# Kernel tuning notes

Hardware: AMD Instinct MI355X
Metric: run time of the kernel (lower is better)

## Reference

```python
import jax, jax.numpy as jnp
import numpy as np

B, S, D, H, DH, R = 8, 2048, 1024, 16, 64, 32
ALPHA, BETA, GAMMA = 0.2, 0.1, 0.1


def setup_inputs() -> dict:
    key = jax.random.key(0)
    ks = jax.random.split(key, 5)
    x = jax.random.normal(ks[0], (B, S, D), jnp.float32)
    q = jax.random.normal(ks[1], (B, S, H, DH), jnp.float32)
    k = jax.random.normal(ks[2], (B, S, H, DH), jnp.float32)
    v_value = jax.random.normal(ks[3], (B, S, D), jnp.float32)
    # reentry_proj weight (orthogonal init approximated by scaled gaussian)
    W = jax.random.normal(ks[4], (D, D), jnp.float32) * np.float32(np.sqrt(0.5 / D))
    return {"x": x, "q": q, "k": k, "v_value": v_value, "W": W}


def _normalize(t):
    return t / (jnp.linalg.norm(t, axis=-1, keepdims=True) + 1e-6)


def reference(x, q, k, v_value, W):
    Bz, Sl, Dm = x.shape
    qf = q.reshape(Bz, Sl, Dm).transpose(1, 0, 2)        # (S, B, D)
    kf = k.reshape(Bz, Sl, Dm).transpose(1, 0, 2)        # (S, B, D)
    vf = v_value.transpose(1, 0, 2)                      # (S, B, D)
    U0 = jnp.zeros((Bz, R, Dm), x.dtype)
    V0 = jnp.zeros((Bz, R, Dm), x.dtype)

    def step(carry, inp):
        U, V = carry
        q_t, k_t, v_t = inp                              # each (B, D)
        U = (1.0 - ALPHA) * U + ALPHA * _normalize(q_t)[:, None, :]
        V = (1.0 - ALPHA) * V + ALPHA * _normalize(k_t)[:, None, :]
        # y_t = (U^T V) v_t, computed factorized: never materialize dim x dim
        s = jnp.einsum('brd,bd->br', V, v_t)             # (B, R)
        y = jnp.einsum('brd,br->bd', U, s)               # (B, D)
        n = jnp.maximum(jnp.linalg.norm(y, axis=-1, keepdims=True), 1e-6)
        y = y / (1.0 + BETA * (n - 1.0))                 # homeostasis
        fb = GAMMA * (y @ W.T)                           # reentry projection
        return (U, V), fb

    (_, _), fbs = jax.lax.scan(step, (U0, V0), (qf, kf, vf))
    return x + fbs.transpose(1, 0, 2)                    # (B, S, D)
```

## Files before the change

### kernel.cpp

```cpp
#include <hip/hip_runtime.h>
#include <hip/hip_bf16.h>
#include <cstdint>
#include <cstddef>

#define B_ 8
#define S_ 2048
#define D_ 1024
#define RFAC 32.0f
#define ALPHA 0.2f
#define BETA 0.1f
#define GAMMA 0.1f
#define KW 32
#define TB 64
#define PF_ 8

typedef float f32x4_t __attribute__((ext_vector_type(4)));
typedef short bf16x8_t __attribute__((ext_vector_type(8)));

__device__ __forceinline__ unsigned short f2bf(float f) {
    unsigned u = __float_as_uint(f);
    u = (u + 0x7fffu + ((u >> 16) & 1u)) >> 16;
    return (unsigned short)u;
}
__device__ __forceinline__ float bf2f(unsigned short h) {
    return __uint_as_float(((unsigned)h) << 16);
}

__global__ __launch_bounds__(256) void wconv_k(const float* __restrict__ W,
                                               unsigned short* __restrict__ Wb) {
    int i = blockIdx.x * 256 + threadIdx.x;
    float4 w = ((const float4*)W)[i];
    ushort4 o;
    o.x = f2bf(w.x); o.y = f2bf(w.y); o.z = f2bf(w.z); o.w = f2bf(w.w);
    ((ushort4*)Wb)[i] = o;
}

__global__ __launch_bounds__(256) void ema_fused_k(const float* __restrict__ q,
                                                   const float* __restrict__ kk,
                                                   const float* __restrict__ vv,
                                                   unsigned short* __restrict__ Ub,
                                                   float* __restrict__ coef) {
    __shared__ float smn[2][8];
    __shared__ float sm2[TB * 8];
    const int chunks = S_ / TB;
    int b  = blockIdx.x / chunks;
    int t0 = (blockIdx.x % chunks) * TB;
    int ts = t0 - KW; if (ts < 0) ts = 0;
    int tid = threadIdx.x;
    int lane = tid & 63, wave = tid >> 6;
    size_t bbase = (size_t)b * S_ * D_ + tid * 4;
    const float* qp = q + bbase;
    const float* kp = kk + bbase;
    const float* vp = vv + bbase;
    unsigned short* up = Ub + bbase;

    float4 pq[PF_], pk[PF_], pv[PF_];
#pragma unroll
    for (int j = 0; j < PF_; ++j) {
        size_t o = (size_t)(ts + j) * D_;
        pq[j] = *(const float4*)(qp + o);
        pk[j] = *(const float4*)(kp + o);
        if (ts + j >= t0) pv[j] = *(const float4*)(vp + o);
    }
    float u0 = 0.f, u1 = 0.f, u2 = 0.f, u3 = 0.f;
    float v0 = 0.f, v1 = 0.f, v2 = 0.f, v3 = 0.f;
    const float om = 1.f - ALPHA;
    const int NI = t0 + TB - ts;
    const int tend = t0 + TB;
    for (int g = 0; g < NI; g += PF_) {
#pragma unroll
        for (int j = 0; j < PF_; ++j) {
            int t = ts + g + j;
            int slot = t & 1;
            float sqq = pq[j].x * pq[j].x + pq[j].y * pq[j].y
                      + pq[j].z * pq[j].z + pq[j].w * pq[j].w;
            float sqk = pk[j].x * pk[j].x + pk[j].y * pk[j].y
                      + pk[j].z * pk[j].z + pk[j].w * pk[j].w;
#pragma unroll
            for (int off = 32; off > 0; off >>= 1) {
                sqq += __shfl_xor(sqq, off, 64);
                sqk += __shfl_xor(sqk, off, 64);
            }
            if (lane == 0) {
                smn[slot][wave * 2 + 0] = sqq;
                smn[slot][wave * 2 + 1] = sqk;
            }
            asm volatile("s_waitcnt lgkmcnt(0)" ::: "memory");
            __builtin_amdgcn_s_barrier();
            asm volatile("" ::: "memory");
            float nq = smn[slot][0] + smn[slot][2] + smn[slot][4] + smn[slot][6];
            float nk = smn[slot][1] + smn[slot][3] + smn[slot][5] + smn[slot][7];
            float aq = ALPHA / (sqrtf(nq) + 1e-6f);
            float ak = ALPHA / (sqrtf(nk) + 1e-6f);
            u0 = om * u0 + aq * pq[j].x; u1 = om * u1 + aq * pq[j].y;
            u2 = om * u2 + aq * pq[j].z; u3 = om * u3 + aq * pq[j].w;
            v0 = om * v0 + ak * pk[j].x; v1 = om * v1 + ak * pk[j].y;
            v2 = om * v2 + ak * pk[j].z; v3 = om * v3 + ak * pk[j].w;
            if (t >= t0) {
                float uu = u0 * u0 + u1 * u1 + u2 * u2 + u3 * u3;
                float sd = v0 * pv[j].x + v1 * pv[j].y + v2 * pv[j].z + v3 * pv[j].w;
#pragma unroll
                for (int off = 32; off > 0; off >>= 1) {
                    uu += __shfl_xor(uu, off, 64);
                    sd += __shfl_xor(sd, off, 64);
                }
                if (lane == 0) {
                    sm2[(t - t0) * 8 + wave * 2 + 0] = uu;
                    sm2[(t - t0) * 8 + wave * 2 + 1] = sd;
                }
                ushort4 us;
                us.x = f2bf(u0); us.y = f2bf(u1); us.z = f2bf(u2); us.w = f2bf(u3);
                *(ushort4*)(up + (size_t)t * D_) = us;
            }
            int tf = t + PF_;
            int tc = tf < tend ? tf : tend - 1;
            size_t o2 = (size_t)tc * D_;
            pq[j] = *(const float4*)(qp + o2);
            pk[j] = *(const float4*)(kp + o2);
            if (tf >= t0) pv[j] = *(const float4*)(vp + o2);
        }
    }
    __syncthreads();
    if (tid < TB) {
        float uu = sm2[tid * 8 + 0] + sm2[tid * 8 + 2] + sm2[tid * 8 + 4] + sm2[tid * 8 + 6];
        float sd = sm2[tid * 8 + 1] + sm2[tid * 8 + 3] + sm2[tid * 8 + 5] + sm2[tid * 8 + 7];
        float nrm = RFAC * fabsf(sd) * sqrtf(uu);
        float n = fmaxf(nrm, 1e-6f);
        coef[b * S_ + t0 + tid] = GAMMA * RFAC * sd / (1.f + BETA * (n - 1.f));
    }
}

#define BM 128
#define BN 128
#define BK 64
#define NT (D_ / BK)

__global__ __launch_bounds__(256) void gemm_k(const unsigned short* __restrict__ A,
                                              const unsigned short* __restrict__ Bw,
                                              const float* __restrict__ coef,
                                              const float* __restrict__ x,
                                              float* __restrict__ out) {
    const int N = D_, K = D_;
    __shared__ unsigned short lds[2 * 2 * BM * BK];
    int bid = blockIdx.x;
    int swz = (bid & 7) * 128 + (bid >> 3);
    int tm = swz >> 3, tn = swz & 7;
    int m0 = tm * BM, n0 = tn * BN;
    int tid = threadIdx.x;
    int lane = tid & 63;
    int wid = tid >> 6;
    int wr = wid >> 1, wc = wid & 1;
    int lr = lane & 15, lg = lane >> 4;

    f32x4_t acc[4][4];
#pragma unroll
    for (int i = 0; i < 4; ++i)
#pragma unroll
        for (int j = 0; j < 4; ++j)
            acc[i][j] = (f32x4_t){0.f, 0.f, 0.f, 0.f};

#define STAGE_MAT(buf, kt, isB)                                                       \
    {                                                                                 \
        const unsigned short* Gp =                                                    \
            ((isB) ? Bw + (size_t)n0 * K : A + (size_t)m0 * K) + (size_t)(kt) * BK;   \
        char* Lp = (char*)lds + (buf) * 32768 + (isB) * 16384;                        \
        _Pragma("unroll")                                                             \
        for (int i = 0; i < 4; ++i) {                                                 \
            int c = i * 256 + tid;                                                    \
            int row = c >> 3, cl = c & 7;                                             \
            int gc = cl ^ (row & 7);                   \
            __builtin_amdgcn_global_load_lds(                                         \
                (const __attribute__((address_space(1))) void*)(Gp + (size_t)row * K + gc * 8), \
                (__attribute__((address_space(3))) void*)(Lp + c * 16), 16, 0, 0);    \
        }                                                                             \
    }
#define STAGE_TILE(buf, kt) STAGE_MAT(buf, kt, 0) STAGE_MAT(buf, kt, 1)

    STAGE_TILE(0, 0);
    STAGE_TILE(1, 1);

    for (int t = 0; t < NT; ++t) {
        if (t == NT - 1) asm volatile("s_waitcnt vmcnt(0)" ::: "memory");
        else             asm volatile("s_waitcnt vmcnt(8)" ::: "memory");
        __builtin_amdgcn_s_barrier();
        const unsigned short* La = lds + (t & 1) * 16384;
        const unsigned short* Lb = La + 8192;
        bf16x8_t af[4][2], bf[4][2];
#pragma unroll
        for (int kkk = 0; kkk < 2; ++kkk) {
#pragma unroll
            for (int mi = 0; mi < 4; ++mi) {
                int row = wr * 64 + mi * 16 + lr;
                int ch = (kkk * 4 + lg) ^ (row & 7);
                af[mi][kkk] = *(const bf16x8_t*)(La + (row * 8 + ch) * 8);
            }
#pragma unroll
            for (int ni = 0; ni < 4; ++ni) {
                int row = wc * 64 + ni * 16 + lr;
                int ch = (kkk * 4 + lg) ^ (row & 7);
                bf[ni][kkk] = *(const bf16x8_t*)(Lb + (row * 8 + ch) * 8);
            }
        }
        asm volatile("s_waitcnt lgkmcnt(0)" ::: "memory");
        __builtin_amdgcn_sched_barrier(0);
        __builtin_amdgcn_s_setprio(1);
#pragma unroll
        for (int kkk = 0; kkk < 2; ++kkk)
#pragma unroll
            for (int mi = 0; mi < 4; ++mi)
#pragma unroll
                for (int ni = 0; ni < 4; ++ni)
                    acc[mi][ni] = __builtin_amdgcn_mfma_f32_16x16x32_bf16(
                        af[mi][kkk], bf[ni][kkk], acc[mi][ni], 0, 0, 0);
        __builtin_amdgcn_s_setprio(0);
        __builtin_amdgcn_s_barrier();
        if (t + 2 < NT) { STAGE_TILE((t & 1), t + 2); }
    }
#undef STAGE_TILE
#undef STAGE_MAT

#pragma unroll
    for (int mi = 0; mi < 4; ++mi) {
#pragma unroll
        for (int i = 0; i < 4; ++i) {
            int m = m0 + wr * 64 + mi * 16 + lg * 4 + i;
            float cf = coef[m];
#pragma unroll
            for (int ni = 0; ni < 4; ++ni) {
                int n = n0 + wc * 64 + ni * 16 + lr;
                size_t idx = (size_t)m * N + n;
                out[idx] = x[idx] + cf * acc[mi][ni][i];
            }
        }
    }
}

extern "C" void kernel_launch(void* const* d_in, const int* in_sizes, int n_in,
                              void* d_out, int out_size, void* d_ws, size_t ws_size,
                              hipStream_t stream) {
    const float* x  = (const float*)d_in[0];
    const float* q  = (const float*)d_in[1];
    const float* k  = (const float*)d_in[2];
    const float* vv = (const float*)d_in[3];
    const float* W  = (const float*)d_in[4];
    float* out = (float*)d_out;

    const size_t M = (size_t)B_ * S_;
    char* ws = (char*)d_ws;
    unsigned short* Ub = (unsigned short*)ws;
    unsigned short* Wb = (unsigned short*)(ws + M * D_ * 2);
    float* coef = (float*)(ws + M * D_ * 2 + (size_t)D_ * D_ * 2);
    size_t needed = M * D_ * 2 + (size_t)D_ * D_ * 2 + M * 4;
    if (ws_size < needed) return;

    wconv_k<<<dim3((D_ * D_) / 1024), dim3(256), 0, stream>>>(W, Wb);
    ema_fused_k<<<dim3(B_ * (S_ / TB)), dim3(256), 0, stream>>>(q, k, vv, Ub, coef);
    gemm_k<<<dim3((M / BM) * (D_ / BN)), dim3(256), 0, stream>>>(Ub, Wb, coef, x, out);
}
```

Measured before the change: 139.0 us.

## Compute EMA norms ahead of use and defer per-step reductions to LDS

```diff
diff --git a/kernel.cpp b/kernel.cpp
--- a/kernel.cpp
+++ b/kernel.cpp
@@ -13,6 +13,7 @@
 #define KW 32
 #define TB 64
 #define PF_ 8
+#define NS 4
 
 typedef float f32x4_t __attribute__((ext_vector_type(4)));
 typedef short bf16x8_t __attribute__((ext_vector_type(8)));
@@ -21,9 +22,6 @@
     unsigned u = __float_as_uint(f);
     u = (u + 0x7fffu + ((u >> 16) & 1u)) >> 16;
     return (unsigned short)u;
-}
-__device__ __forceinline__ float bf2f(unsigned short h) {
-    return __uint_as_float(((unsigned)h) << 16);
 }
 
 __global__ __launch_bounds__(256) void wconv_k(const float* __restrict__ W,
@@ -40,8 +38,8 @@
                                                    const float* __restrict__ vv,
                                                    unsigned short* __restrict__ Ub,
                                                    float* __restrict__ coef) {
-    __shared__ float smn[2][8];
-    __shared__ float sm2[TB * 8];
+    __shared__ float smn[8][8];
+    __shared__ float pp[TB][256][2];
     const int chunks = S_ / TB;
     int b  = blockIdx.x / chunks;
     int t0 = (blockIdx.x % chunks) * TB;
@@ -53,6 +51,7 @@
     const float* kp = kk + bbase;
     const float* vp = vv + bbase;
     unsigned short* up = Ub + bbase;
+    const int tend = t0 + TB;
 
     float4 pq[PF_], pk[PF_], pv[PF_];
 #pragma unroll
@@ -62,52 +61,60 @@
         pk[j] = *(const float4*)(kp + o);
         if (ts + j >= t0) pv[j] = *(const float4*)(vp + o);
     }
-    float u0 = 0.f, u1 = 0.f, u2 = 0.f, u3 = 0.f;
-    float v0 = 0.f, v1 = 0.f, v2 = 0.f, v3 = 0.f;
+#pragma unroll
+    for (int j = 0; j < NS; ++j) {
+        float sqq = pq[j].x*pq[j].x + pq[j].y*pq[j].y + pq[j].z*pq[j].z + pq[j].w*pq[j].w;
+        float sqk = pk[j].x*pk[j].x + pk[j].y*pk[j].y + pk[j].z*pk[j].z + pk[j].w*pk[j].w;
+#pragma unroll
+        for (int off = 32; off > 0; off >>= 1) {
+            sqq += __shfl_xor(sqq, off, 64);
+            sqk += __shfl_xor(sqk, off, 64);
+        }
+        if (lane == 0) {
+            smn[(ts + j) & 7][wave * 2 + 0] = sqq;
+            smn[(ts + j) & 7][wave * 2 + 1] = sqk;
+        }
+    }
+    __syncthreads();
+
+    float u0=0.f,u1=0.f,u2=0.f,u3=0.f,v0=0.f,v1=0.f,v2=0.f,v3=0.f;
     const float om = 1.f - ALPHA;
-    const int NI = t0 + TB - ts;
-    const int tend = t0 + TB;
+    const int NI = tend - ts;
     for (int g = 0; g < NI; g += PF_) {
 #pragma unroll
         for (int j = 0; j < PF_; ++j) {
             int t = ts + g + j;
-            int slot = t & 1;
-            float sqq = pq[j].x * pq[j].x + pq[j].y * pq[j].y
-                      + pq[j].z * pq[j].z + pq[j].w * pq[j].w;
-            float sqk = pk[j].x * pk[j].x + pk[j].y * pk[j].y
-                      + pk[j].z * pk[j].z + pk[j].w * pk[j].w;
-#pragma unroll
-            for (int off = 32; off > 0; off >>= 1) {
-                sqq += __shfl_xor(sqq, off, 64);
-                sqk += __shfl_xor(sqk, off, 64);
-            }
-            if (lane == 0) {
-                smn[slot][wave * 2 + 0] = sqq;
-                smn[slot][wave * 2 + 1] = sqk;
-            }
             asm volatile("s_waitcnt lgkmcnt(0)" ::: "memory");
             __builtin_amdgcn_s_barrier();
-            asm volatile("" ::: "memory");
-            float nq = smn[slot][0] + smn[slot][2] + smn[slot][4] + smn[slot][6];
-            float nk = smn[slot][1] + smn[slot][3] + smn[slot][5] + smn[slot][7];
+            int tN = t + NS;
+            if (tN < tend) {
+                int sN = (j + NS) & 7;
+                float4 aN = pq[sN], bN = pk[sN];
+                float sqq = aN.x*aN.x + aN.y*aN.y + aN.z*aN.z + aN.w*aN.w;
+                float sqk = bN.x*bN.x + bN.y*bN.y + bN.z*bN.z + bN.w*bN.w;
+#pragma unroll
+                for (int off = 32; off > 0; off >>= 1) {
+                    sqq += __shfl_xor(sqq, off, 64);
+                    sqk += __shfl_xor(sqk, off, 64);
+                }
+                if (lane == 0) {
+                    smn[tN & 7][wave * 2 + 0] = sqq;
+                    smn[tN & 7][wave * 2 + 1] = sqk;
+                }
+            }
+            float4 s0 = *(const float4*)&smn[t & 7][0];
+            float4 s1 = *(const float4*)&smn[t & 7][4];
+            float nq = s0.x + s0.z + s1.x + s1.z;
+            float nk = s0.y + s0.w + s1.y + s1.w;
             float aq = ALPHA / (sqrtf(nq) + 1e-6f);
             float ak = ALPHA / (sqrtf(nk) + 1e-6f);
-            u0 = om * u0 + aq * pq[j].x; u1 = om * u1 + aq * pq[j].y;
-            u2 = om * u2 + aq * pq[j].z; u3 = om * u3 + aq * pq[j].w;
-            v0 = om * v0 + ak * pk[j].x; v1 = om * v1 + ak * pk[j].y;
-            v2 = om * v2 + ak * pk[j].z; v3 = om * v3 + ak * pk[j].w;
+            u0 = om*u0 + aq*pq[j].x; u1 = om*u1 + aq*pq[j].y;
+            u2 = om*u2 + aq*pq[j].z; u3 = om*u3 + aq*pq[j].w;
+            v0 = om*v0 + ak*pk[j].x; v1 = om*v1 + ak*pk[j].y;
+            v2 = om*v2 + ak*pk[j].z; v3 = om*v3 + ak*pk[j].w;
             if (t >= t0) {
-                float uu = u0 * u0 + u1 * u1 + u2 * u2 + u3 * u3;
-                float sd = v0 * pv[j].x + v1 * pv[j].y + v2 * pv[j].z + v3 * pv[j].w;
-#pragma unroll
-                for (int off = 32; off > 0; off >>= 1) {
-                    uu += __shfl_xor(uu, off, 64);
-                    sd += __shfl_xor(sd, off, 64);
-                }
-                if (lane == 0) {
-                    sm2[(t - t0) * 8 + wave * 2 + 0] = uu;
-                    sm2[(t - t0) * 8 + wave * 2 + 1] = sd;
-                }
+                pp[t - t0][tid][0] = u0*u0 + u1*u1 + u2*u2 + u3*u3;
+                pp[t - t0][tid][1] = v0*pv[j].x + v1*pv[j].y + v2*pv[j].z + v3*pv[j].w;
                 ushort4 us;
                 us.x = f2bf(u0); us.y = f2bf(u1); us.z = f2bf(u2); us.w = f2bf(u3);
                 *(ushort4*)(up + (size_t)t * D_) = us;
@@ -121,12 +128,22 @@
         }
     }
     __syncthreads();
-    if (tid < TB) {
-        float uu = sm2[tid * 8 + 0] + sm2[tid * 8 + 2] + sm2[tid * 8 + 4] + sm2[tid * 8 + 6];
-        float sd = sm2[tid * 8 + 1] + sm2[tid * 8 + 3] + sm2[tid * 8 + 5] + sm2[tid * 8 + 7];
-        float nrm = RFAC * fabsf(sd) * sqrtf(uu);
-        float n = fmaxf(nrm, 1e-6f);
-        coef[b * S_ + t0 + tid] = GAMMA * RFAC * sd / (1.f + BETA * (n - 1.f));
+    for (int tt = wave; tt < TB; tt += 4) {
+        const float* row = &pp[tt][lane * 4][0];
+        float4 r0 = *(const float4*)(row);
+        float4 r1 = *(const float4*)(row + 4);
+        float uu = r0.x + r0.z + r1.x + r1.z;
+        float sd = r0.y + r0.w + r1.y + r1.w;
+#pragma unroll
+        for (int off = 32; off > 0; off >>= 1) {
+            uu += __shfl_xor(uu, off, 64);
+            sd += __shfl_xor(sd, off, 64);
+        }
+        if (lane == 0) {
+            float nrm = RFAC * fabsf(sd) * sqrtf(uu);
+            float n = fmaxf(nrm, 1e-6f);
+            coef[b * S_ + t0 + tt] = GAMMA * RFAC * sd / (1.f + BETA * (n - 1.f));
+        }
     }
 }
 
```

Result: no change. 138.4 us (-0.4%).
